# Kernel tuning notes

Hardware: AMD Instinct MI355X
Metric: run time of the kernel (lower is better)

The kernel has to match this reference:

```python
import jax, jax.numpy as jnp
import numpy as np

NUM_NODES = 12
NUM_EDGES = 30
OUT_CH = 32
HID = 192
B = 8192
FEAT = 2 * (NUM_NODES - 1)            # 22
N = B * NUM_NODES                      # 98304 nodes
E = B * NUM_EDGES                      # 245760 edges
OUT_SPACE = NUM_NODES ** 2 - NUM_NODES # 132


def setup_inputs() -> dict:
    key = jax.random.key(0)
    ks = jax.random.split(key, 16)
    def p(k, shape, fan):
        return jax.random.normal(k, shape, dtype=jnp.float32) / np.float32(np.sqrt(fan))
    return {
        "x": jax.random.normal(ks[0], (N, FEAT), dtype=jnp.float32),
        "edge_attr": jax.random.normal(ks[1], (E, NUM_EDGES), dtype=jnp.float32),
        "edge_index": jax.random.randint(ks[2], (2, E), 0, N, dtype=jnp.int64) if jax.config.jax_enable_x64 else jax.random.randint(ks[2], (2, E), 0, N, dtype=jnp.int32),
        "mlp1_w1": p(ks[3], (NUM_EDGES, HID), NUM_EDGES),
        "mlp1_b1": jnp.zeros((HID,), jnp.float32),
        "mlp1_w2": p(ks[4], (HID, FEAT * OUT_CH), HID),
        "mlp1_b2": jnp.zeros((FEAT * OUT_CH,), jnp.float32),
        "root1": p(ks[5], (FEAT, OUT_CH), FEAT),
        "bias1": jnp.zeros((OUT_CH,), jnp.float32),
        "lin1_w": p(ks[6], (NUM_NODES * OUT_CH, 96), NUM_NODES * OUT_CH),
        "lin1_b": jnp.zeros((96,), jnp.float32),
        "lin2_w": p(ks[7], (96, 48), 96),
        "lin2_b": jnp.zeros((48,), jnp.float32),
        "lin3_w": p(ks[8], (48, OUT_SPACE), 48),
        "lin3_b": jnp.zeros((OUT_SPACE,), jnp.float32),
    }


def reference(x, edge_attr, edge_index, mlp1_w1, mlp1_b1, mlp1_w2, mlp1_b2,
              root1, bias1, lin1_w, lin1_b, lin2_w, lin2_b, lin3_w, lin3_b):
    src, dst = edge_index[0], edge_index[1]
    # Edge-MLP ('Understanding'): produces a [FEAT, OUT_CH] weight per edge
    h = jax.nn.relu(edge_attr @ mlp1_w1 + mlp1_b1)               # [E, HID]
    W = (h @ mlp1_w2 + mlp1_b2).reshape(-1, FEAT, OUT_CH)        # [E, 22, 32]
    # NNConv: gather source features, per-edge matmul, scatter-add to dst
    msg = jnp.einsum('ec,eco->eo', x[src], W)                    # [E, 32]
    agg = jax.ops.segment_sum(msg, dst, num_segments=x.shape[0]) # [N, 32]
    g = jax.nn.relu(x @ root1 + agg + bias1)                     # conv1 + ReLU
    # Dense head
    g = g.reshape(-1, NUM_NODES * OUT_CH)                        # [B, 384]
    g = jax.nn.relu(g @ lin1_w + lin1_b)
    g = jax.nn.relu(g @ lin2_w + lin2_b)
    g = jax.nn.relu(g @ lin3_w + lin3_b)                         # [B, 132]
    return g
```

## Files before the change

kernel.cpp:

```cpp
#include <hip/hip_runtime.h>
#include <hip/hip_bf16.h>

typedef short s8v __attribute__((ext_vector_type(8)));
typedef float f4v __attribute__((ext_vector_type(4)));

#define MFMA16(A,B,C) __builtin_amdgcn_mfma_f32_16x16x32_bf16((A),(B),(C),0,0,0)

#define E_TOT 245760
#define N_TOT 98304
#define B_GR  8192

__device__ __forceinline__ unsigned short f2bf(float f) {
    unsigned u = __builtin_bit_cast(unsigned, f);
    u += 0x7fffu + ((u >> 16) & 1u);
    return (unsigned short)(u >> 16);
}

__device__ __forceinline__ void gload_lds16(const void* g, void* l) {
    __builtin_amdgcn_global_load_lds(
        (const __attribute__((address_space(1))) void*)g,
        (__attribute__((address_space(3))) void*)l, 16, 0, 0);
}

__global__ void pack_kernel(const float* __restrict__ w1, const float* __restrict__ w2,
                            const float* __restrict__ l1w, const float* __restrict__ l2w,
                            const float* __restrict__ l3w,
                            unsigned short* __restrict__ w1p, unsigned short* __restrict__ w2p,
                            unsigned short* __restrict__ l1p, unsigned short* __restrict__ l2p,
                            unsigned short* __restrict__ l3p)
{
    int idx = blockIdx.x * 256 + threadIdx.x;
    if (idx >= 192000) return;
    if (idx < 6144) {
        int i = idx & 7, l = (idx >> 3) & 63, nt = idx >> 9;
        int k = (l >> 4) * 8 + i, col = nt * 16 + (l & 15);
        w1p[idx] = f2bf(k < 30 ? w1[k * 192 + col] : 0.f);
    } else if (idx < 141312) {
        int e = idx - 6144;
        int i = e & 7, l = (e >> 3) & 63, rest = e >> 9;
        int s = rest % 6, ct = rest / 6, t = ct & 1, c = ct >> 1;
        int k = s * 32 + (l >> 4) * 8 + i, j = c * 32 + t * 16 + (l & 15);
        w2p[e] = f2bf(w2[k * 704 + j]);
    } else if (idx < 178176) {
        int e = idx - 141312;
        int i = e & 7, l = (e >> 3) & 63, rest = e >> 9;
        int s = rest % 12, nt = rest / 12;
        int k = s * 32 + (l >> 4) * 8 + i, j = nt * 16 + (l & 15);
        l1p[e] = f2bf(l1w[k * 96 + j]);
    } else if (idx < 182784) {
        int e = idx - 178176;
        int i = e & 7, l = (e >> 3) & 63, rest = e >> 9;
        int s = rest % 3, nt = rest / 3;
        int k = s * 32 + (l >> 4) * 8 + i, j = nt * 16 + (l & 15);
        l2p[e] = f2bf(l2w[k * 48 + j]);
    } else {
        int e = idx - 182784;
        int i = e & 7, l = (e >> 3) & 63, rest = e >> 9;
        int s = rest & 1, nt = rest >> 1;
        int k = s * 32 + (l >> 4) * 8 + i, j = nt * 16 + (l & 15);
        l3p[e] = f2bf((k < 48 && j < 132) ? l3w[k * 132 + j] : 0.f);
    }
}

__launch_bounds__(256, 2)
__global__ void edge_kernel(const float* __restrict__ x,
                            const float* __restrict__ ea,
                            const int*   __restrict__ eidx,
                            const unsigned short* __restrict__ w1p,
                            const unsigned short* __restrict__ w2p,
                            const float* __restrict__ b1,
                            const float* __restrict__ b2,
                            float* __restrict__ agg)
{
    __shared__ __align__(16) unsigned short w2cl[6144];
    __shared__ __align__(16) unsigned short hscr[4][16][200];
    __shared__ float xs[192][22];
    __shared__ float b2l[704];
    __shared__ int   dstl[192];

    const int tid  = threadIdx.x;
    const int wave = tid >> 6, lane = tid & 63;
    const int hi = lane >> 4, col = lane & 15;
    const int e0 = blockIdx.x * 192;

    for (int idx = tid; idx < 192 * 22; idx += 256) {
        int e = idx / 22, c = idx - e * 22;
        int s = eidx[e0 + e];
        xs[e][c] = x[s * 22 + c];
    }
    for (int idx = tid; idx < 192; idx += 256) dstl[idx] = eidx[E_TOT + e0 + idx];
    for (int idx = tid; idx < 704; idx += 256) b2l[idx] = b2[idx];

    s8v w1f[12];
#pragma unroll
    for (int nt = 0; nt < 12; ++nt) w1f[nt] = *(const s8v*)(w1p + (nt * 64 + lane) * 8);
    float b1v[12];
#pragma unroll
    for (int nt = 0; nt < 12; ++nt) b1v[nt] = b1[nt * 16 + col];

    s8v haf[3][6];
#pragma unroll
    for (int mt = 0; mt < 3; ++mt) {
        int er = e0 + wave * 48 + mt * 16 + col;
        s8v af;
#pragma unroll
        for (int i = 0; i < 8; ++i) {
            int k = hi * 8 + i;
            af[i] = (short)f2bf(k < 30 ? ea[er * 30 + k] : 0.f);
        }
        f4v hc[12];
#pragma unroll
        for (int nt = 0; nt < 12; ++nt) {
            f4v z = {0.f, 0.f, 0.f, 0.f};
            hc[nt] = MFMA16(af, w1f[nt], z);
        }
        __syncthreads();
#pragma unroll
        for (int nt = 0; nt < 12; ++nt)
#pragma unroll
            for (int r = 0; r < 4; ++r) {
                float v = hc[nt][r] + b1v[nt];
                v = v > 0.f ? v : 0.f;
                hscr[wave][hi * 4 + r][nt * 16 + col] = f2bf(v);
            }
        __syncthreads();
#pragma unroll
        for (int s = 0; s < 6; ++s)
            haf[mt][s] = *(const s8v*)&hscr[wave][col][s * 32 + hi * 8];
    }

    f4v msg[3][2];
#pragma unroll
    for (int mt = 0; mt < 3; ++mt)
#pragma unroll
        for (int t = 0; t < 2; ++t) msg[mt][t] = (f4v){0.f, 0.f, 0.f, 0.f};

    for (int c = 0; c < 22; ++c) {
        __syncthreads();
#pragma unroll
        for (int r = 0; r < 3; ++r) {
            const unsigned short* g = w2p + c * 6144 + (r * 256 + tid) * 8;
            unsigned short* l = &w2cl[(r * 256 + wave * 64) * 8];
            gload_lds16(g, l);
        }
        __syncthreads();

        s8v bf[2][6];
#pragma unroll
        for (int t = 0; t < 2; ++t)
#pragma unroll
            for (int s = 0; s < 6; ++s)
                bf[t][s] = *(const s8v*)&w2cl[((t * 6 + s) * 64 + lane) * 8];

        f4v pacc[3][2];
#pragma unroll
        for (int mt = 0; mt < 3; ++mt)
#pragma unroll
            for (int t = 0; t < 2; ++t) {
                f4v a = {0.f, 0.f, 0.f, 0.f};
#pragma unroll
                for (int s = 0; s < 6; ++s) a = MFMA16(haf[mt][s], bf[t][s], a);
                pacc[mt][t] = a;
            }

        float b2v0 = b2l[c * 32 + col];
        float b2v1 = b2l[c * 32 + 16 + col];
#pragma unroll
        for (int mt = 0; mt < 3; ++mt)
#pragma unroll
            for (int r = 0; r < 4; ++r) {
                float xv = xs[wave * 48 + mt * 16 + hi * 4 + r][c];
                msg[mt][0][r] += xv * (pacc[mt][0][r] + b2v0);
                msg[mt][1][r] += xv * (pacc[mt][1][r] + b2v1);
            }
    }

#pragma unroll
    for (int mt = 0; mt < 3; ++mt)
#pragma unroll
        for (int r = 0; r < 4; ++r) {
            int e = wave * 48 + mt * 16 + hi * 4 + r;
            int d = dstl[e];
            atomicAdd(&agg[d * 32 + col],      msg[mt][0][r]);
            atomicAdd(&agg[d * 32 + 16 + col], msg[mt][1][r]);
        }
}

__global__ void node_kernel(const float* __restrict__ x, const float* __restrict__ agg,
                            const float* __restrict__ root1, const float* __restrict__ bias1,
                            unsigned short* __restrict__ g2d)
{
    __shared__ float r1[704];
    int tid = threadIdx.x;
    for (int i = tid; i < 704; i += 256) r1[i] = root1[i];
    __syncthreads();
    int gid = blockIdx.x * 256 + tid;
    int n = gid >> 2, j0 = (gid & 3) * 8;
    float acc[8];
#pragma unroll
    for (int j = 0; j < 8; ++j) acc[j] = agg[n * 32 + j0 + j] + bias1[j0 + j];
    for (int c = 0; c < 22; ++c) {
        float xc = x[n * 22 + c];
#pragma unroll
        for (int j = 0; j < 8; ++j) acc[j] += xc * r1[c * 32 + j0 + j];
    }
    s8v v;
#pragma unroll
    for (int j = 0; j < 8; ++j) {
        float t = acc[j] > 0.f ? acc[j] : 0.f;
        v[j] = (short)f2bf(t);
    }
    *(s8v*)&g2d[n * 32 + j0] = v;
}

__launch_bounds__(256)
__global__ void head1_kernel(const unsigned short* __restrict__ g2d,
                             const unsigned short* __restrict__ l1p,
                             const float* __restrict__ bias, unsigned short* __restrict__ a1)
{
    int tid = threadIdx.x, wave = tid >> 6, lane = tid & 63, hi = lane >> 4, col = lane & 15;
    int r0 = blockIdx.x * 128 + wave * 32;
    f4v acc[2][6];
#pragma unroll
    for (int m = 0; m < 2; ++m)
#pragma unroll
        for (int n = 0; n < 6; ++n) acc[m][n] = (f4v){0.f, 0.f, 0.f, 0.f};
    for (int s = 0; s < 12; ++s) {
        s8v a0 = *(const s8v*)&g2d[(r0 + col) * 384 + s * 32 + hi * 8];
        s8v a1f = *(const s8v*)&g2d[(r0 + 16 + col) * 384 + s * 32 + hi * 8];
#pragma unroll
        for (int nt = 0; nt < 6; ++nt) {
            s8v bfr = *(const s8v*)&l1p[((nt * 12 + s) * 64 + lane) * 8];
            acc[0][nt] = MFMA16(a0, bfr, acc[0][nt]);
            acc[1][nt] = MFMA16(a1f, bfr, acc[1][nt]);
        }
    }
#pragma unroll
    for (int nt = 0; nt < 6; ++nt) {
        float bv = bias[nt * 16 + col];
#pragma unroll
        for (int m = 0; m < 2; ++m)
#pragma unroll
            for (int r = 0; r < 4; ++r) {
                float v = acc[m][nt][r] + bv;
                v = v > 0.f ? v : 0.f;
                a1[(r0 + m * 16 + hi * 4 + r) * 96 + nt * 16 + col] = f2bf(v);
            }
    }
}

__launch_bounds__(256)
__global__ void head2_kernel(const unsigned short* __restrict__ a1,
                             const unsigned short* __restrict__ l2p,
                             const float* __restrict__ bias, unsigned short* __restrict__ a2)
{
    int tid = threadIdx.x, wave = tid >> 6, lane = tid & 63, hi = lane >> 4, col = lane & 15;
    int r0 = blockIdx.x * 128 + wave * 32;
    f4v acc[2][3];
#pragma unroll
    for (int m = 0; m < 2; ++m)
#pragma unroll
        for (int n = 0; n < 3; ++n) acc[m][n] = (f4v){0.f, 0.f, 0.f, 0.f};
#pragma unroll
    for (int s = 0; s < 3; ++s) {
        s8v a0 = *(const s8v*)&a1[(r0 + col) * 96 + s * 32 + hi * 8];
        s8v a1f = *(const s8v*)&a1[(r0 + 16 + col) * 96 + s * 32 + hi * 8];
#pragma unroll
        for (int nt = 0; nt < 3; ++nt) {
            s8v bfr = *(const s8v*)&l2p[((nt * 3 + s) * 64 + lane) * 8];
            acc[0][nt] = MFMA16(a0, bfr, acc[0][nt]);
            acc[1][nt] = MFMA16(a1f, bfr, acc[1][nt]);
        }
    }
#pragma unroll
    for (int nt = 0; nt < 3; ++nt) {
        float bv = bias[nt * 16 + col];
#pragma unroll
        for (int m = 0; m < 2; ++m)
#pragma unroll
            for (int r = 0; r < 4; ++r) {
                float v = acc[m][nt][r] + bv;
                v = v > 0.f ? v : 0.f;
                a2[(r0 + m * 16 + hi * 4 + r) * 48 + nt * 16 + col] = f2bf(v);
            }
    }
}

__launch_bounds__(256)
__global__ void head3_kernel(const unsigned short* __restrict__ a2,
                             const unsigned short* __restrict__ l3p,
                             const float* __restrict__ bias, float* __restrict__ out)
{
    int tid = threadIdx.x, wave = tid >> 6, lane = tid & 63, hi = lane >> 4, col = lane & 15;
    int r0 = blockIdx.x * 128 + wave * 32;
    f4v acc[2][9];
#pragma unroll
    for (int m = 0; m < 2; ++m)
#pragma unroll
        for (int n = 0; n < 9; ++n) acc[m][n] = (f4v){0.f, 0.f, 0.f, 0.f};
#pragma unroll
    for (int s = 0; s < 2; ++s) {
        s8v a0, a1f;
        if (s == 1 && hi >= 2) {
            a0 = (s8v)0; a1f = (s8v)0;
        } else {
            a0 = *(const s8v*)&a2[(r0 + col) * 48 + s * 32 + hi * 8];
            a1f = *(const s8v*)&a2[(r0 + 16 + col) * 48 + s * 32 + hi * 8];
        }
#pragma unroll
        for (int nt = 0; nt < 9; ++nt) {
            s8v bfr = *(const s8v*)&l3p[((nt * 2 + s) * 64 + lane) * 8];
            acc[0][nt] = MFMA16(a0, bfr, acc[0][nt]);
            acc[1][nt] = MFMA16(a1f, bfr, acc[1][nt]);
        }
    }
#pragma unroll
    for (int nt = 0; nt < 9; ++nt) {
        int oc = nt * 16 + col;
        if (oc < 132) {
            float bv = bias[oc];
#pragma unroll
            for (int m = 0; m < 2; ++m)
#pragma unroll
                for (int r = 0; r < 4; ++r) {
                    float v = acc[m][nt][r] + bv;
                    v = v > 0.f ? v : 0.f;
                    out[(r0 + m * 16 + hi * 4 + r) * 132 + oc] = v;
                }
        }
    }
}

extern "C" void kernel_launch(void* const* d_in, const int* in_sizes, int n_in,
                              void* d_out, int out_size, void* d_ws, size_t ws_size,
                              hipStream_t stream)
{
    const float* x     = (const float*)d_in[0];
    const float* ea    = (const float*)d_in[1];
    const int*   ei    = (const int*)d_in[2];
    const float* w1    = (const float*)d_in[3];
    const float* b1    = (const float*)d_in[4];
    const float* w2    = (const float*)d_in[5];
    const float* b2    = (const float*)d_in[6];
    const float* root1 = (const float*)d_in[7];
    const float* bias1 = (const float*)d_in[8];
    const float* l1w   = (const float*)d_in[9];
    const float* l1b   = (const float*)d_in[10];
    const float* l2w   = (const float*)d_in[11];
    const float* l2b   = (const float*)d_in[12];
    const float* l3w   = (const float*)d_in[13];
    const float* l3b   = (const float*)d_in[14];
    float* out = (float*)d_out;

    char* ws = (char*)d_ws;
    unsigned short* w1p = (unsigned short*)(ws + 0);
    unsigned short* w2p = (unsigned short*)(ws + 12288);
    unsigned short* l1p = (unsigned short*)(ws + 282624);
    unsigned short* l2p = (unsigned short*)(ws + 356352);
    unsigned short* l3p = (unsigned short*)(ws + 365568);
    float*          agg = (float*)(ws + 384000);
    unsigned short* g2d = (unsigned short*)(ws + 12966912);
    unsigned short* a1  = (unsigned short*)(ws + 19258368);
    unsigned short* a2  = (unsigned short*)(ws + 20831232);

    hipMemsetAsync(agg, 0, (size_t)N_TOT * 32 * 4, stream);
    pack_kernel<<<750, 256, 0, stream>>>(w1, w2, l1w, l2w, l3w, w1p, w2p, l1p, l2p, l3p);
    edge_kernel<<<1280, 256, 0, stream>>>(x, ea, ei, w1p, w2p, b1, b2, agg);
    node_kernel<<<1536, 256, 0, stream>>>(x, agg, root1, bias1, g2d);
    head1_kernel<<<64, 256, 0, stream>>>(g2d, l1p, l1b, a1);
    head2_kernel<<<64, 256, 0, stream>>>(a1, l2p, l2b, a2);
    head3_kernel<<<64, 256, 0, stream>>>(a2, l3p, l3b, out);
}
```

Baseline: 226.2 us.

## Double-buffer W2 chunks, shrink edge LDS, MFMA node kernel, fuse head kernels

The edge kernel now double-buffers the per-channel W2 slices in LDS so the next chunk's global-to-LDS load overlaps the current MFMAs, halving barriers per channel. It also aliases hscr with the W2 buffer, stores gathered x as bf16, and raises the occupancy hint to 4 blocks per CU. Bias is folded into the MFMA accumulator init. The node kernel is rewritten to use MFMA for x@root1, and the three head kernels are fused into one that keeps intermediates in LDS, with bf16 x adding rounding error.

```diff
diff --git a/kernel.cpp b/kernel.cpp
--- a/kernel.cpp
+++ b/kernel.cpp
@@ -8,14 +8,18 @@
 
 #define E_TOT 245760
 #define N_TOT 98304
-#define B_GR  8192
 
 __device__ __forceinline__ unsigned short f2bf(float f) {
     unsigned u = __builtin_bit_cast(unsigned, f);
     u += 0x7fffu + ((u >> 16) & 1u);
     return (unsigned short)(u >> 16);
 }
-
+__device__ __forceinline__ float bflo(unsigned u) {
+    return __builtin_bit_cast(float, u << 16);
+}
+__device__ __forceinline__ float bfhi(unsigned u) {
+    return __builtin_bit_cast(float, u & 0xffff0000u);
+}
 __device__ __forceinline__ void gload_lds16(const void* g, void* l) {
     __builtin_amdgcn_global_load_lds(
         (const __attribute__((address_space(1))) void*)g,
@@ -62,7 +66,7 @@
     }
 }
 
-__launch_bounds__(256, 2)
+__launch_bounds__(256, 4)
 __global__ void edge_kernel(const float* __restrict__ x,
                             const float* __restrict__ ea,
                             const int*   __restrict__ eidx,
@@ -72,11 +76,12 @@
                             const float* __restrict__ b2,
                             float* __restrict__ agg)
 {
-    __shared__ __align__(16) unsigned short w2cl[6144];
-    __shared__ __align__(16) unsigned short hscr[4][16][200];
-    __shared__ float xs[192][22];
-    __shared__ float b2l[704];
-    __shared__ int   dstl[192];
+    __shared__ __align__(16) unsigned char smem[38400];
+    unsigned short* w2u  = (unsigned short*)smem;
+    unsigned short* hscr = (unsigned short*)smem;
+    unsigned short* xs   = (unsigned short*)(smem + 25600);
+    float*          b2l  = (float*)(smem + 34816);
+    int*            dstl = (int*)(smem + 37632);
 
     const int tid  = threadIdx.x;
     const int wave = tid >> 6, lane = tid & 63;
@@ -86,7 +91,7 @@
     for (int idx = tid; idx < 192 * 22; idx += 256) {
         int e = idx / 22, c = idx - e * 22;
         int s = eidx[e0 + e];
-        xs[e][c] = x[s * 22 + c];
+        xs[e * 24 + c] = f2bf(x[s * 22 + c]);
     }
     for (int idx = tid; idx < 192; idx += 256) dstl[idx] = eidx[E_TOT + e0 + idx];
     for (int idx = tid; idx < 704; idx += 256) b2l[idx] = b2[idx];
@@ -114,20 +119,25 @@
             f4v z = {0.f, 0.f, 0.f, 0.f};
             hc[nt] = MFMA16(af, w1f[nt], z);
         }
-        __syncthreads();
 #pragma unroll
         for (int nt = 0; nt < 12; ++nt)
 #pragma unroll
             for (int r = 0; r < 4; ++r) {
                 float v = hc[nt][r] + b1v[nt];
                 v = v > 0.f ? v : 0.f;
-                hscr[wave][hi * 4 + r][nt * 16 + col] = f2bf(v);
+                hscr[(wave * 16 + hi * 4 + r) * 200 + nt * 16 + col] = f2bf(v);
             }
-        __syncthreads();
 #pragma unroll
         for (int s = 0; s < 6; ++s)
-            haf[mt][s] = *(const s8v*)&hscr[wave][col][s * 32 + hi * 8];
-    }
+            haf[mt][s] = *(const s8v*)&hscr[(wave * 16 + col) * 200 + s * 32 + hi * 8];
+    }
+
+    __syncthreads();
+
+#pragma unroll
+    for (int r = 0; r < 3; ++r)
+        gload_lds16(w2p + (r * 256 + tid) * 8, w2u + (r * 256 + wave * 64) * 8);
+    __syncthreads();
 
     f4v msg[3][2];
 #pragma unroll
@@ -135,44 +145,86 @@
 #pragma unroll
         for (int t = 0; t < 2; ++t) msg[mt][t] = (f4v){0.f, 0.f, 0.f, 0.f};
 
-    for (int c = 0; c < 22; ++c) {
-        __syncthreads();
-#pragma unroll
-        for (int r = 0; r < 3; ++r) {
-            const unsigned short* g = w2p + c * 6144 + (r * 256 + tid) * 8;
-            unsigned short* l = &w2cl[(r * 256 + wave * 64) * 8];
-            gload_lds16(g, l);
-        }
-        __syncthreads();
-
-        s8v bf[2][6];
-#pragma unroll
-        for (int t = 0; t < 2; ++t)
-#pragma unroll
-            for (int s = 0; s < 6; ++s)
-                bf[t][s] = *(const s8v*)&w2cl[((t * 6 + s) * 64 + lane) * 8];
-
-        f4v pacc[3][2];
+    for (int cp = 0; cp < 11; ++cp) {
+        unsigned xu[12];
 #pragma unroll
         for (int mt = 0; mt < 3; ++mt)
 #pragma unroll
-            for (int t = 0; t < 2; ++t) {
-                f4v a = {0.f, 0.f, 0.f, 0.f};
-#pragma unroll
-                for (int s = 0; s < 6; ++s) a = MFMA16(haf[mt][s], bf[t][s], a);
-                pacc[mt][t] = a;
+            for (int r = 0; r < 4; ++r)
+                xu[mt * 4 + r] = *(const unsigned*)&xs[(wave * 48 + mt * 16 + hi * 4 + r) * 24 + 2 * cp];
+
+        {
+            const int c = 2 * cp;
+#pragma unroll
+            for (int r = 0; r < 3; ++r)
+                gload_lds16(w2p + (c + 1) * 6144 + (r * 256 + tid) * 8,
+                            w2u + 6144 + (r * 256 + wave * 64) * 8);
+            s8v bf[2][6];
+#pragma unroll
+            for (int t = 0; t < 2; ++t)
+#pragma unroll
+                for (int s = 0; s < 6; ++s)
+                    bf[t][s] = *(const s8v*)&w2u[((t * 6 + s) * 64 + lane) * 8];
+            float b2v0 = b2l[c * 32 + col];
+            float b2v1 = b2l[c * 32 + 16 + col];
+            f4v pacc[3][2];
+#pragma unroll
+            for (int mt = 0; mt < 3; ++mt) {
+                pacc[mt][0] = (f4v){b2v0, b2v0, b2v0, b2v0};
+                pacc[mt][1] = (f4v){b2v1, b2v1, b2v1, b2v1};
+#pragma unroll
+                for (int s = 0; s < 6; ++s) {
+                    pacc[mt][0] = MFMA16(haf[mt][s], bf[0][s], pacc[mt][0]);
+                    pacc[mt][1] = MFMA16(haf[mt][s], bf[1][s], pacc[mt][1]);
+                }
             }
-
-        float b2v0 = b2l[c * 32 + col];
-        float b2v1 = b2l[c * 32 + 16 + col];
-#pragma unroll
-        for (int mt = 0; mt < 3; ++mt)
-#pragma unroll
-            for (int r = 0; r < 4; ++r) {
-                float xv = xs[wave * 48 + mt * 16 + hi * 4 + r][c];
-                msg[mt][0][r] += xv * (pacc[mt][0][r] + b2v0);
-                msg[mt][1][r] += xv * (pacc[mt][1][r] + b2v1);
+#pragma unroll
+            for (int mt = 0; mt < 3; ++mt)
+#pragma unroll
+                for (int r = 0; r < 4; ++r) {
+                    float xv = bflo(xu[mt * 4 + r]);
+                    msg[mt][0][r] += xv * pacc[mt][0][r];
+                    msg[mt][1][r] += xv * pacc[mt][1][r];
+                }
+            __syncthreads();
+        }
+        {
+            const int c = 2 * cp + 1;
+            if (c < 21) {
+#pragma unroll
+                for (int r = 0; r < 3; ++r)
+                    gload_lds16(w2p + (c + 1) * 6144 + (r * 256 + tid) * 8,
+                                w2u + (r * 256 + wave * 64) * 8);
             }
+            s8v bf[2][6];
+#pragma unroll
+            for (int t = 0; t < 2; ++t)
+#pragma unroll
+                for (int s = 0; s < 6; ++s)
+                    bf[t][s] = *(const s8v*)&w2u[6144 + ((t * 6 + s) * 64 + lane) * 8];
+            float b2v0 = b2l[c * 32 + col];
+            float b2v1 = b2l[c * 32 + 16 + col];
+            f4v pacc[3][2];
+#pragma unroll
+            for (int mt = 0; mt < 3; ++mt) {
+                pacc[mt][0] = (f4v){b2v0, b2v0, b2v0, b2v0};
+                pacc[mt][1] = (f4v){b2v1, b2v1, b2v1, b2v1};
+#pragma unroll
+                for (int s = 0; s < 6; ++s) {
+                    pacc[mt][0] = MFMA16(haf[mt][s], bf[0][s], pacc[mt][0]);
+                    pacc[mt][1] = MFMA16(haf[mt][s], bf[1][s], pacc[mt][1]);
+                }
+            }
+#pragma unroll
+            for (int mt = 0; mt < 3; ++mt)
+#pragma unroll
+                for (int r = 0; r < 4; ++r) {
+                    float xv = bfhi(xu[mt * 4 + r]);
+                    msg[mt][0][r] += xv * pacc[mt][0][r];
+                    msg[mt][1][r] += xv * pacc[mt][1][r];
+                }
+            __syncthreads();
+        }
     }
 
 #pragma unroll
@@ -186,147 +238,151 @@
         }
 }
 
+__launch_bounds__(256)
 __global__ void node_kernel(const float* __restrict__ x, const float* __restrict__ agg,
                             const float* __restrict__ root1, const float* __restrict__ bias1,
                             unsigned short* __restrict__ g2d)
 {
-    __shared__ float r1[704];
-    int tid = threadIdx.x;
-    for (int i = tid; i < 704; i += 256) r1[i] = root1[i];
-    __syncthreads();
-    int gid = blockIdx.x * 256 + tid;
-    int n = gid >> 2, j0 = (gid & 3) * 8;
-    float acc[8];
-#pragma unroll
-    for (int j = 0; j < 8; ++j) acc[j] = agg[n * 32 + j0 + j] + bias1[j0 + j];
-    for (int c = 0; c < 22; ++c) {
-        float xc = x[n * 22 + c];
-#pragma unroll
-        for (int j = 0; j < 8; ++j) acc[j] += xc * r1[c * 32 + j0 + j];
-    }
-    s8v v;
-#pragma unroll
-    for (int j = 0; j < 8; ++j) {
-        float t = acc[j] > 0.f ? acc[j] : 0.f;
-        v[j] = (short)f2bf(t);
-    }
-    *(s8v*)&g2d[n * 32 + j0] = v;
+    const int tid = threadIdx.x, wave = tid >> 6, lane = tid & 63;
+    const int hi = lane >> 4, col = lane & 15;
+    const int n0 = blockIdx.x * 256 + wave * 64;
+
+    s8v bfr[2];
+#pragma unroll
+    for (int nt = 0; nt < 2; ++nt)
+#pragma unroll
+        for (int i = 0; i < 8; ++i) {
+            int k = hi * 8 + i;
+            bfr[nt][i] = (short)f2bf(k < 22 ? root1[k * 32 + nt * 16 + col] : 0.f);
+        }
+    float bb0 = bias1[col], bb1 = bias1[16 + col];
+
+#pragma unroll
+    for (int mt = 0; mt < 4; ++mt) {
+        int node = n0 + mt * 16 + col;
+        s8v af;
+        if (hi < 2) {
+            const float2* p = (const float2*)&x[node * 22 + hi * 8];
+            float2 t0 = p[0], t1 = p[1], t2 = p[2], t3 = p[3];
+            af[0] = (short)f2bf(t0.x); af[1] = (short)f2bf(t0.y);
+            af[2] = (short)f2bf(t1.x); af[3] = (short)f2bf(t1.y);
+            af[4] = (short)f2bf(t2.x); af[5] = (short)f2bf(t2.y);
+            af[6] = (short)f2bf(t3.x); af[7] = (short)f2bf(t3.y);
+        } else if (hi == 2) {
+            const float2* p = (const float2*)&x[node * 22 + 16];
+            float2 t0 = p[0], t1 = p[1], t2 = p[2];
+            af[0] = (short)f2bf(t0.x); af[1] = (short)f2bf(t0.y);
+            af[2] = (short)f2bf(t1.x); af[3] = (short)f2bf(t1.y);
+            af[4] = (short)f2bf(t2.x); af[5] = (short)f2bf(t2.y);
+            af[6] = 0; af[7] = 0;
+        } else {
+            af = (s8v)0;
+        }
+        f4v c0 = {bb0, bb0, bb0, bb0};
+        f4v c1 = {bb1, bb1, bb1, bb1};
+        c0 = MFMA16(af, bfr[0], c0);
+        c1 = MFMA16(af, bfr[1], c1);
+#pragma unroll
+        for (int r = 0; r < 4; ++r) {
+            int row = n0 + mt * 16 + hi * 4 + r;
+            float v0 = c0[r] + agg[row * 32 + col];
+            float v1 = c1[r] + agg[row * 32 + 16 + col];
+            g2d[row * 32 + col]      = f2bf(v0 > 0.f ? v0 : 0.f);
+            g2d[row * 32 + 16 + col] = f2bf(v1 > 0.f ? v1 : 0.f);
+        }
+    }
 }
 
 __launch_bounds__(256)
-__global__ void head1_kernel(const unsigned short* __restrict__ g2d,
-                             const unsigned short* __restrict__ l1p,
-                             const float* __restrict__ bias, unsigned short* __restrict__ a1)
+__global__ void head_kernel(const unsigned short* __restrict__ g2d,
+                            const unsigned short* __restrict__ l1p,
+                            const unsigned short* __restrict__ l2p,
+                            const unsigned short* __restrict__ l3p,
+                            const float* __restrict__ l1b,
+                            const float* __restrict__ l2b,
+                            const float* __restrict__ l3b,
+                            float* __restrict__ out)
 {
-    int tid = threadIdx.x, wave = tid >> 6, lane = tid & 63, hi = lane >> 4, col = lane & 15;
-    int r0 = blockIdx.x * 128 + wave * 32;
-    f4v acc[2][6];
-#pragma unroll
-    for (int m = 0; m < 2; ++m)
-#pragma unroll
-        for (int n = 0; n < 6; ++n) acc[m][n] = (f4v){0.f, 0.f, 0.f, 0.f};
+    __shared__ __align__(16) unsigned short a1s[4][16][104];
+    __shared__ __align__(16) unsigned short a2s[4][16][56];
+
+    const int tid = threadIdx.x, wave = tid >> 6, lane = tid & 63;
+    const int hi = lane >> 4, col = lane & 15;
+    const int r0 = blockIdx.x * 64 + wave * 16;
+
+    f4v acc1[6];
+#pragma unroll
+    for (int nt = 0; nt < 6; ++nt) {
+        float bv = l1b[nt * 16 + col];
+        acc1[nt] = (f4v){bv, bv, bv, bv};
+    }
+#pragma unroll
     for (int s = 0; s < 12; ++s) {
-        s8v a0 = *(const s8v*)&g2d[(r0 + col) * 384 + s * 32 + hi * 8];
-        s8v a1f = *(const s8v*)&g2d[(r0 + 16 + col) * 384 + s * 32 + hi * 8];
+        s8v a = *(const s8v*)&g2d[(r0 + col) * 384 + s * 32 + hi * 8];
 #pragma unroll
         for (int nt = 0; nt < 6; ++nt) {
-            s8v bfr = *(const s8v*)&l1p[((nt * 12 + s) * 64 + lane) * 8];
-            acc[0][nt] = MFMA16(a0, bfr, acc[0][nt]);
-            acc[1][nt] = MFMA16(a1f, bfr, acc[1][nt]);
-        }
-    }
-#pragma unroll
-    for (int nt = 0; nt < 6; ++nt) {
-        float bv = bias[nt * 16 + col];
-#pragma unroll
-        for (int m = 0; m < 2; ++m)
-#pragma unroll
-            for (int r = 0; r < 4; ++r) {
-                float v = acc[m][nt][r] + bv;
-                v = v > 0.f ? v : 0.f;
-                a1[(r0 + m * 16 + hi * 4 + r) * 96 + nt * 16 + col] = f2bf(v);
-            }
-    }
-}
-
-__launch_bounds__(256)
-__global__ void head2_kernel(const unsigned short* __restrict__ a1,
-                             const unsigned short* __restrict__ l2p,
-                             const float* __restrict__ bias, unsigned short* __restrict__ a2)
-{
-    int tid = threadIdx.x, wave = tid >> 6, lane = tid & 63, hi = lane >> 4, col = lane & 15;
-    int r0 = blockIdx.x * 128 + wave * 32;
-    f4v acc[2][3];
-#pragma unroll
-    for (int m = 0; m < 2; ++m)
-#pragma unroll
-        for (int n = 0; n < 3; ++n) acc[m][n] = (f4v){0.f, 0.f, 0.f, 0.f};
+            s8v b = *(const s8v*)&l1p[((nt * 12 + s) * 64 + lane) * 8];
+            acc1[nt] = MFMA16(a, b, acc1[nt]);
+        }
+    }
+#pragma unroll
+    for (int nt = 0; nt < 6; ++nt)
+#pragma unroll
+        for (int r = 0; r < 4; ++r) {
+            float v = acc1[nt][r];
+            a1s[wave][hi * 4 + r][nt * 16 + col] = f2bf(v > 0.f ? v : 0.f);
+        }
+
+    f4v acc2[3];
+#pragma unroll
+    for (int nt = 0; nt < 3; ++nt) {
+        float bv = l2b[nt * 16 + col];
+        acc2[nt] = (f4v){bv, bv, bv, bv};
+    }
 #pragma unroll
     for (int s = 0; s < 3; ++s) {
-        s8v a0 = *(const s8v*)&a1[(r0 + col) * 96 + s * 32 + hi * 8];
-        s8v a1f = *(const s8v*)&a1[(r0 + 16 + col) * 96 + s * 32 + hi * 8];
+        s8v a = *(const s8v*)&a1s[wave][col][s * 32 + hi * 8];
 #pragma unroll
         for (int nt = 0; nt < 3; ++nt) {
-            s8v bfr = *(const s8v*)&l2p[((nt * 3 + s) * 64 + lane) * 8];
-            acc[0][nt] = MFMA16(a0, bfr, acc[0][nt]);
-            acc[1][nt] = MFMA16(a1f, bfr, acc[1][nt]);
-        }
-    }
-#pragma unroll
-    for (int nt = 0; nt < 3; ++nt) {
-        float bv = bias[nt * 16 + col];
-#pragma unroll
-        for (int m = 0; m < 2; ++m)
-#pragma unroll
-            for (int r = 0; r < 4; ++r) {
-                float v = acc[m][nt][r] + bv;
-                v = v > 0.f ? v : 0.f;
-                a2[(r0 + m * 16 + hi * 4 + r) * 48 + nt * 16 + col] = f2bf(v);
-            }
-    }
-}
-
-__launch_bounds__(256)
-__global__ void head3_kernel(const unsigned short* __restrict__ a2,
-                             const unsigned short* __restrict__ l3p,
-                             const float* __restrict__ bias, float* __restrict__ out)
-{
-    int tid = threadIdx.x, wave = tid >> 6, lane = tid & 63, hi = lane >> 4, col = lane & 15;
-    int r0 = blockIdx.x * 128 + wave * 32;
-    f4v acc[2][9];
-#pragma unroll
-    for (int m = 0; m < 2; ++m)
-#pragma unroll
-        for (int n = 0; n < 9; ++n) acc[m][n] = (f4v){0.f, 0.f, 0.f, 0.f};
+            s8v b = *(const s8v*)&l2p[((nt * 3 + s) * 64 + lane) * 8];
+            acc2[nt] = MFMA16(a, b, acc2[nt]);
+        }
+    }
+#pragma unroll
+    for (int nt = 0; nt < 3; ++nt)
+#pragma unroll
+        for (int r = 0; r < 4; ++r) {
+            float v = acc2[nt][r];
+            a2s[wave][hi * 4 + r][nt * 16 + col] = f2bf(v > 0.f ? v : 0.f);
+        }
+
+    f4v acc3[9];
+#pragma unroll
+    for (int nt = 0; nt < 9; ++nt) {
+        int oc = nt * 16 + col;
+        float bv = oc < 132 ? l3b[oc] : 0.f;
+        acc3[nt] = (f4v){bv, bv, bv, bv};
+    }
 #pragma unroll
     for (int s = 0; s < 2; ++s) {
-        s8v a0, a1f;
-        if (s == 1 && hi >= 2) {
-            a0 = (s8v)0; a1f = (s8v)0;
-        } else {
-            a0 = *(const s8v*)&a2[(r0 + col) * 48 + s * 32 + hi * 8];
-            a1f = *(const s8v*)&a2[(r0 + 16 + col) * 48 + s * 32 + hi * 8];
-        }
+        s8v a;
+        if (s == 1 && hi >= 2) a = (s8v)0;
+        else a = *(const s8v*)&a2s[wave][col][s * 32 + hi * 8];
 #pragma unroll
         for (int nt = 0; nt < 9; ++nt) {
-            s8v bfr = *(const s8v*)&l3p[((nt * 2 + s) * 64 + lane) * 8];
-            acc[0][nt] = MFMA16(a0, bfr, acc[0][nt]);
-            acc[1][nt] = MFMA16(a1f, bfr, acc[1][nt]);
+            s8v b = *(const s8v*)&l3p[((nt * 2 + s) * 64 + lane) * 8];
+            acc3[nt] = MFMA16(a, b, acc3[nt]);
         }
     }
 #pragma unroll
     for (int nt = 0; nt < 9; ++nt) {
         int oc = nt * 16 + col;
         if (oc < 132) {
-            float bv = bias[oc];
-#pragma unroll
-            for (int m = 0; m < 2; ++m)
-#pragma unroll
-                for (int r = 0; r < 4; ++r) {
-                    float v = acc[m][nt][r] + bv;
-                    v = v > 0.f ? v : 0.f;
-                    out[(r0 + m * 16 + hi * 4 + r) * 132 + oc] = v;
-                }
+#pragma unroll
+            for (int r = 0; r < 4; ++r) {
+                float v = acc3[nt][r];
+                out[(r0 + hi * 4 + r) * 132 + oc] = v > 0.f ? v : 0.f;
+            }
         }
     }
 }
@@ -360,14 +416,10 @@
     unsigned short* l3p = (unsigned short*)(ws + 365568);
     float*          agg = (float*)(ws + 384000);
     unsigned short* g2d = (unsigned short*)(ws + 12966912);
-    unsigned short* a1  = (unsigned short*)(ws + 19258368);
-    unsigned short* a2  = (unsigned short*)(ws + 20831232);
 
     hipMemsetAsync(agg, 0, (size_t)N_TOT * 32 * 4, stream);
     pack_kernel<<<750, 256, 0, stream>>>(w1, w2, l1w, l2w, l3w, w1p, w2p, l1p, l2p, l3p);
     edge_kernel<<<1280, 256, 0, stream>>>(x, ea, ei, w1p, w2p, b1, b2, agg);
-    node_kernel<<<1536, 256, 0, stream>>>(x, agg, root1, bias1, g2d);
-    head1_kernel<<<64, 256, 0, stream>>>(g2d, l1p, l1b, a1);
-    head2_kernel<<<64, 256, 0, stream>>>(a1, l2p, l2b, a2);
-    head3_kernel<<<64, 256, 0, stream>>>(a2, l3p, l3b, out);
-}
+    node_kernel<<<384, 256, 0, stream>>>(x, agg, root1, bias1, g2d);
+    head_kernel<<<128, 256, 0, stream>>>(g2d, l1p, l2p, l3p, l1b, l2b, l3b, out);
+}
```

Result: slower. 414.7 us (+83.3%).
